# Kernel optimization log

Measured on AMD Instinct MI355X. Metric: run time of the kernel, lower is better.

## Reference

```python
import jax, jax.numpy as jnp
import numpy as np

MASK_RADIUS = 30.0

def _lowpass_mask(H, W):
    cht, cwt = H // 2, W // 2
    fy = jnp.arange(H, dtype=jnp.float32)[:, None]
    fx = jnp.arange(W, dtype=jnp.float32)[None, :]
    dist = jnp.sqrt((fx - cwt) ** 2 + (fy - cht) ** 2)
    return (dist <= MASK_RADIUS).astype(jnp.float32)

def setup_inputs() -> dict:
    key = jax.random.key(0)
    k1, k2, k3 = jax.random.split(key, 3)
    x = jax.random.normal(k1, (16, 64, 128, 128), dtype=jnp.float32)
    weight = jax.random.normal(k2, (64, 64, 3, 3), dtype=jnp.float32)
    bias = jax.random.normal(k3, (64,), dtype=jnp.float32)
    return {"x": x, "weight": weight, "bias": bias}

def reference(x, weight, bias):
    B, Cin, H, W = x.shape
    # torch.fft.fftshift default shifts ALL dims; jnp default matches.
    fft_x = jnp.fft.fftshift(jnp.fft.fft2(x))                    # [B,Cin,H,W] complex
    kernel_fft = jnp.fft.fftshift(jnp.fft.fft2(weight, s=(H, W)))  # [Cout,Cin,H,W] complex
    # low-pass filter in the shifted frequency domain
    fft_x = fft_x * _lowpass_mask(H, W)
    # channel mixing = batched complex GEMM per frequency (avoids [B,Cout,Cin,H,W] intermediate)
    fft_out = jnp.einsum('bihw,oihw->bohw', fft_x, kernel_fft)
    out = jnp.fft.ifft2(jnp.fft.ifftshift(fft_out, axes=(-2, -1)), axes=(-2, -1)).real
    return out + bias[None, :, None, None]
```

## Files before the change

### kernel.cpp

```cpp
#include <hip/hip_runtime.h>


#define PI2_128 0.04908738521234052f
#define NF 1891

typedef __attribute__((ext_vector_type(8))) short bf16x8;
typedef __attribute__((ext_vector_type(4))) float f32x4;

__device__ const int k_flist[64] = {
    2, 6, 10, 14, 18, 22, 26, 30, 34, 38, 42, 46, 50, 54, 58,
    3, 7, 11, 15, 19, 23, 27, 31, 35, 39, 43, 47, 51, 55, 59,
    0, 4, 8, 12, 16, 20, 24, 28, 32, 36, 40, 44, 48, 52, 56, 60,
    1, 5, 9, 13, 17, 21, 25, 29, 33, 37, 41, 45, 49, 53, 57,
    0, 0, 0};

__device__ inline unsigned bf16_rne(float v) {
  unsigned u = __float_as_uint(v);
  return (u + 0x7FFFu + ((u >> 16) & 1u)) >> 16;
}

__device__ inline bf16x8 mk_bf16x8(unsigned a, unsigned b, unsigned c, unsigned d) {
  union { unsigned u[4]; bf16x8 v; } x;
  x.u[0] = a; x.u[1] = b; x.u[2] = c; x.u[3] = d;
  return x.v;
}

__global__ __launch_bounds__(256) void k0_what(const float* __restrict__ w,
                                               unsigned* __restrict__ Wt) {
  const int tid = threadIdx.x;
  const int fxp = blockIdx.x >> 4;
  const int ig = blockIdx.x & 15;
  const int il = tid & 3;
  const int o = ((tid >> 5) << 3) | ((tid >> 2) & 7);
  const int i = ig * 4 + il;
  const int op = (o + 32) & 63;
  const float* wp = w + (size_t)(op * 64 + i) * 9;
  float w9[9];
#pragma unroll
  for (int k = 0; k < 9; ++k) w9[k] = wp[k];

  const float fx = (float)(fxp - 30);
  float sn, cs;
  __sincosf(fx * PI2_128, &sn, &cs);
  const float e1x = cs, e1y = -sn;
  const float e2x = e1x * e1x - e1y * e1y, e2y = 2.f * e1x * e1y;
  float rxr[3], rxi[3];
#pragma unroll
  for (int ky = 0; ky < 3; ++ky) {
    rxr[ky] = w9[ky * 3] + w9[ky * 3 + 1] * e1x + w9[ky * 3 + 2] * e2x;
    rxi[ky] = w9[ky * 3 + 1] * e1y + w9[ky * 3 + 2] * e2y;
  }
  float pyx = 1.f, pyy = 0.f;
  const float stx = 0.9987954562f, sty = -0.04906767433f;
  unsigned* Wb = Wt + (size_t)(fxp * 31) * 4096 + (o >> 3) * 512 + (i >> 4) * 128 +
                 (((i >> 2) & 3) * 8 + (o & 7)) * 4 + (i & 3);
  for (int fy = 0; fy < 31; ++fy) {
    float p2x = pyx * pyx - pyy * pyy, p2y = 2.f * pyx * pyy;
    float Wre = rxr[0] + (rxr[1] * pyx - rxi[1] * pyy) + (rxr[2] * p2x - rxi[2] * p2y);
    float Wim = rxi[0] + (rxr[1] * pyy + rxi[1] * pyx) + (rxr[2] * p2y + rxi[2] * p2x);
    Wb[(size_t)fy * 4096] = bf16_rne(Wre) | (bf16_rne(Wim) << 16);
    float nx = pyx * stx - pyy * sty;
    pyy = pyx * sty + pyy * stx;
    pyx = nx;
  }
}

__global__ __launch_bounds__(256) void k12_fwd(const float* __restrict__ x,
                                               float* __restrict__ X2) {
  __shared__ __align__(16) float Cls[8968];
  const int bi = blockIdx.x;
  const int tid = threadIdx.x;
  const float* img = x + (size_t)bi * 16384;

  {
    const int tg = tid >> 5;
    const int xg = tid & 31;
    const int t_[4] = {4 * tg, 4 * tg + 2, 2 * tg + 1, 2 * tg + 17};
    const float sgn = (tg & 1) ? 1.f : -1.f;
    float pc[4], ps[4], stc[4], sts[4];
#pragma unroll
    for (int f = 0; f < 4; ++f) {
      __sincosf((float)t_[f] * PI2_128, &sts[f], &stc[f]);
      pc[f] = 1.f;
      ps[f] = 0.f;
    }
    float ar_[4][4] = {{0.f}}, ai_[4][4] = {{0.f}};
    for (int y = 0; y < 32; ++y) {
      float v[4][4];
#pragma unroll
      for (int k = 0; k < 4; ++k)
#pragma unroll
        for (int m = 0; m < 4; ++m) v[k][m] = img[(y + 32 * k) * 128 + xg + 32 * m];
#pragma unroll
      for (int m = 0; m < 4; ++m) {
        float s = v[0][m] + v[2][m], d = v[0][m] - v[2][m];
        float s2 = v[1][m] + v[3][m], d2 = (v[1][m] - v[3][m]) * sgn;
        float a0 = s + s2, a1 = s - s2;
        ar_[0][m] += a0 * pc[0];
        ai_[0][m] -= a0 * ps[0];
        ar_[1][m] += a1 * pc[1];
        ai_[1][m] -= a1 * ps[1];
        ar_[2][m] += d * pc[2] + d2 * ps[2];
        ai_[2][m] += -d * ps[2] + d2 * pc[2];
        ar_[3][m] += d * pc[3] + d2 * ps[3];
        ai_[3][m] += -d * ps[3] + d2 * pc[3];
      }
#pragma unroll
      for (int f = 0; f < 4; ++f) {
        float c = pc[f], s = ps[f];
        pc[f] = c * stc[f] - s * sts[f];
        ps[f] = s * stc[f] + c * sts[f];
      }
    }
#pragma unroll
    for (int f = 0; f < 4; ++f) {
      int t = t_[f];
      float Ar = ar_[f][0] + ar_[f][2], Ai = ai_[f][0] + ai_[f][2];
      float Br = ar_[f][0] - ar_[f][2], Bi = ai_[f][0] - ai_[f][2];
      float Cr = ar_[f][1] + ar_[f][3], Ci = ai_[f][1] + ai_[f][3];
      float Dr = ar_[f][1] - ar_[f][3], Di = ai_[f][1] - ai_[f][3];
      float* base = Cls + xg * 70 + 2 * t;
      *(float2*)(base + 0 * 2244) = make_float2(Ar + Cr, Ai + Ci);
      *(float2*)(base + 1 * 2244) = make_float2(Br + Di, Bi - Dr);
      *(float2*)(base + 2 * 2244) = make_float2(Ar - Cr, Ai - Ci);
      *(float2*)(base + 3 * 2244) = make_float2(Br - Di, Bi + Dr);
    }
  }
  __syncthreads();

  {
    const int tg2 = tid >> 5;
    const int fxg = tid & 31;
    float accr[2][4] = {{0.f}}, acci[2][4] = {{0.f}};
    int fxp_[2], r_[2];
    float pc2[2], ps2[2], stc2[2], sts2[2];
#pragma unroll
    for (int u = 0; u < 2; ++u) {
      fxp_[u] = k_flist[2 * fxg + u];
      r_[u] = (fxp_[u] + 2) & 3;
      float fx = (float)(fxp_[u] - 30);
      __sincosf(fx * PI2_128, &sts2[u], &stc2[u]);
      pc2[u] = 1.f;
      ps2[u] = 0.f;
    }
    for (int xx = 0; xx < 32; ++xx) {
#pragma unroll
      for (int u = 0; u < 2; ++u) {
        const float* bp = Cls + r_[u] * 2244 + xx * 70 + 8 * tg2;
        float2 p0 = *(const float2*)(bp);
        float2 p1 = *(const float2*)(bp + 2);
        float2 p2 = *(const float2*)(bp + 4);
        float2 p3 = *(const float2*)(bp + 6);
        float zr[4] = {p0.x, p1.x, p2.x, p3.x};
        float zi[4] = {p0.y, p1.y, p2.y, p3.y};
        float c = pc2[u], s = ps2[u];
#pragma unroll
        for (int tt = 0; tt < 4; ++tt) {
          accr[u][tt] += zr[tt] * c + zi[tt] * s;
          acci[u][tt] += zi[tt] * c - zr[tt] * s;
        }
        pc2[u] = c * stc2[u] - s * sts2[u];
        ps2[u] = s * stc2[u] + c * sts2[u];
      }
    }
    float2* X2c = (float2*)X2 + (size_t)bi * NF;
#pragma unroll
    for (int u = 0; u < 2; ++u) {
      if (2 * fxg + u >= 61) continue;
      int fxp = fxp_[u], fx = fxp - 30;
#pragma unroll
      for (int tt = 0; tt < 4; ++tt) {
        int t = 4 * tg2 + tt;
        if (t >= 31) continue;
        bool keep = (t * t + fx * fx) <= 900;
        X2c[fxp * 31 + t] =
            keep ? make_float2(accr[u][tt], acci[u][tt]) : make_float2(0.f, 0.f);
      }
    }
  }
}

__global__ __launch_bounds__(256) void k3_mfma(const float* __restrict__ X2,
                                               const unsigned* __restrict__ WtB,
                                               float* __restrict__ F) {
  const int nwg = (int)gridDim.x;
  const int orig = (int)blockIdx.x;
  const int xcd = orig & 7;
  const int q = nwg >> 3, r = nwg & 7;
  const int blk = (xcd < r ? xcd * (q + 1) : r * (q + 1) + (xcd - r) * q) + (orig >> 3);

  const int tid = (int)threadIdx.x;
  const int wv = tid >> 6;
  const int g = blk * 4 + wv;
  const int f2 = g >> 1;
  if (f2 >= NF) return;
  const int half = g & 1;
  const int lane = tid & 63;
  const int m = lane & 15;
  const int lg = lane >> 4;
  const int bs = (m + 8) & 15;
  const int co = m & 1;

  float2 xv[4][4];
  const float2* Xc = (const float2*)X2;
#pragma unroll
  for (int ks = 0; ks < 4; ++ks)
#pragma unroll
    for (int t = 0; t < 4; ++t)
      xv[ks][t] = Xc[(size_t)(bs * 64 + ks * 16 + lg * 4 + t) * NF + f2];

  unsigned ahi[4][4], alo[4][4];
#pragma unroll
  for (int ks = 0; ks < 4; ++ks) {
#pragma unroll
    for (int t = 0; t < 4; ++t) {
      float xr = xv[ks][t].x, xi = xv[ks][t].y;
      unsigned hr = bf16_rne(xr), hi2 = bf16_rne(xi);
      float lr = xr - __uint_as_float(hr << 16);
      float li = xi - __uint_as_float(hi2 << 16);
      ahi[ks][t] = hr | (hi2 << 16);
      alo[ks][t] = bf16_rne(lr) | (bf16_rne(li) << 16);
    }
  }

  f32x4 acc[4];
#pragma unroll
  for (int nt = 0; nt < 4; ++nt) acc[nt] = {0.f, 0.f, 0.f, 0.f};

  const unsigned* Wb =
      WtB + (size_t)f2 * 4096 + half * 2048 + (lg * 8 + (m >> 1)) * 4;
#pragma unroll
  for (int ks = 0; ks < 4; ++ks) {
    bf16x8 bfr[4];
#pragma unroll
    for (int nt = 0; nt < 4; ++nt) {
      uint4 wq = *(const uint4*)(Wb + nt * 512 + ks * 128);
      unsigned b0, b1, b2, b3;
      if (co) {
        b0 = (wq.x >> 16) | (wq.x << 16);
        b1 = (wq.y >> 16) | (wq.y << 16);
        b2 = (wq.z >> 16) | (wq.z << 16);
        b3 = (wq.w >> 16) | (wq.w << 16);
      } else {
        b0 = wq.x ^ 0x80000000u;
        b1 = wq.y ^ 0x80000000u;
        b2 = wq.z ^ 0x80000000u;
        b3 = wq.w ^ 0x80000000u;
      }
      bfr[nt] = mk_bf16x8(b0, b1, b2, b3);
    }
    bf16x8 ah = mk_bf16x8(ahi[ks][0], ahi[ks][1], ahi[ks][2], ahi[ks][3]);
    bf16x8 al = mk_bf16x8(alo[ks][0], alo[ks][1], alo[ks][2], alo[ks][3]);
#pragma unroll
    for (int nt = 0; nt < 4; ++nt)
      acc[nt] = __builtin_amdgcn_mfma_f32_16x16x32_bf16(ah, bfr[nt], acc[nt], 0, 0, 0);
#pragma unroll
    for (int nt = 0; nt < 4; ++nt)
      acc[nt] = __builtin_amdgcn_mfma_f32_16x16x32_bf16(al, bfr[nt], acc[nt], 0, 0, 0);
  }

  float* Fo = F + (size_t)f2 * 2048 + half * 64 + m;
#pragma unroll
  for (int nt = 0; nt < 4; ++nt)
#pragma unroll
    for (int rr = 0; rr < 4; ++rr)
      Fo[(lg * 4 + rr) * 128 + nt * 16] = acc[nt][rr];
}

__global__ __launch_bounds__(256) void k45_out(const float* __restrict__ F,
                                               const float* __restrict__ bias,
                                               float* __restrict__ out) {
  __shared__ __align__(16) float2 tw[128];
  __shared__ __align__(16) float U[61 * 132];
  __shared__ __align__(16) float TF[3904];
  const int b = blockIdx.x >> 6;
  const int o = blockIdx.x & 63;
  const int tid = threadIdx.x;
  float2* Fl = (float2*)TF;
  const float2* Fc = (const float2*)F + (size_t)(b * 64 + o);
  if (tid < 128) {
    float sv, cv;
    __sincosf((float)tid * PI2_128, &sv, &cv);
    tw[tid] = make_float2(cv, sv);
  }
  for (int j = tid; j < NF; j += 256) Fl[j] = Fc[(size_t)j * 1024];
  __syncthreads();

  {
    const int fy = tid & 31;
    const int xg = tid >> 3 >> 2;
    if (fy < 31) {
      float Sr[4][4] = {{0.f}}, Si[4][4] = {{0.f}};
      float pr[4], pi[4], cr[4], ci[4];
#pragma unroll
      for (int j = 0; j < 4; ++j) {
        int xj = 4 * xg + j;
        float2 st = tw[xj];
        cr[j] = st.x;
        ci[j] = st.y;
        float2 p0 = tw[(-30 * xj) & 127];
        pr[j] = p0.x;
        pi[j] = p0.y;
      }
      const float2* Frow = Fl + fy;
      for (int f4 = 0; f4 < 60; f4 += 4) {
#pragma unroll
        for (int ss = 0; ss < 4; ++ss) {
          const int r = (ss + 2) & 3;
          float2 fv = Frow[(f4 + ss) * 31];
#pragma unroll
          for (int j = 0; j < 4; ++j) {
            Sr[r][j] += fv.x * pr[j] - fv.y * pi[j];
            Si[r][j] += fv.x * pi[j] + fv.y * pr[j];
            float np = pr[j] * cr[j] - pi[j] * ci[j];
            pi[j] = pi[j] * cr[j] + pr[j] * ci[j];
            pr[j] = np;
          }
        }
      }
      {
        float2 fv = Frow[60 * 31];
#pragma unroll
        for (int j = 0; j < 4; ++j) {
          Sr[2][j] += fv.x * pr[j] - fv.y * pi[j];
          Si[2][j] += fv.x * pi[j] + fv.y * pr[j];
        }
      }
#pragma unroll
      for (int j = 0; j < 4; ++j) {
        int xj = 4 * xg + j;
        float Er = Sr[0][j] + Sr[2][j], Ei = Si[0][j] + Si[2][j];
        float Fr = Sr[0][j] - Sr[2][j], Fi = Si[0][j] - Si[2][j];
        float Gr = Sr[1][j] + Sr[3][j], Gi = Si[1][j] + Si[3][j];
        float Hr = Sr[1][j] - Sr[3][j], Hi = Si[1][j] - Si[3][j];
        U[fy * 132 + xj] = Er + Gr;
        U[fy * 132 + xj + 32] = Fr - Hi;
        U[fy * 132 + xj + 64] = Er - Gr;
        U[fy * 132 + xj + 96] = Fr + Hi;
        if (fy >= 1) {
          U[(30 + fy) * 132 + xj] = Ei + Gi;
          U[(30 + fy) * 132 + xj + 32] = Fi + Hr;
          U[(30 + fy) * 132 + xj + 64] = Ei - Gi;
          U[(30 + fy) * 132 + xj + 96] = Fi - Hr;
        }
      }
    }
  }
  __syncthreads();
  {
    const float sc1 = 1.f / 16384.f;
    float* T = TF;
    for (int j = tid; j < 61 * 64; j += 256) {
      int c = j >> 6, y = j & 63;
      float val;
      if (c == 0) val = sc1;
      else if (c <= 30) val = 2.f * sc1 * tw[(c * y) & 127].x;
      else val = -2.f * sc1 * tw[((c - 30) * y) & 127].y;
      T[j] = val;
    }
  }
  __syncthreads();
  {
    const float* T = TF;
    const int yg = tid >> 5;
    const int xg = tid & 31;
    const int y0 = yg * 8, x0 = xg * 4;
    float Pa[8][4] = {{0.f}}, Qa[8][4] = {{0.f}};
    for (int c = 0; c < 60; c += 2) {
      float tf0[8], tf1[8], uf0[4], uf1[4];
      *(float4*)&tf0[0] = *(const float4*)(&T[c * 64 + y0]);
      *(float4*)&tf0[4] = *(const float4*)(&T[c * 64 + y0 + 4]);
      *(float4*)&tf1[0] = *(const float4*)(&T[(c + 1) * 64 + y0]);
      *(float4*)&tf1[4] = *(const float4*)(&T[(c + 1) * 64 + y0 + 4]);
      *(float4*)&uf0[0] = *(const float4*)(&U[c * 132 + x0]);
      *(float4*)&uf1[0] = *(const float4*)(&U[(c + 1) * 132 + x0]);
#pragma unroll
      for (int jy = 0; jy < 8; ++jy)
#pragma unroll
        for (int jx = 0; jx < 4; ++jx) {
          Pa[jy][jx] += tf0[jy] * uf0[jx];
          Qa[jy][jx] += tf1[jy] * uf1[jx];
        }
    }
    {
      float tf0[8], uf0[4];
      *(float4*)&tf0[0] = *(const float4*)(&T[60 * 64 + y0]);
      *(float4*)&tf0[4] = *(const float4*)(&T[60 * 64 + y0 + 4]);
      *(float4*)&uf0[0] = *(const float4*)(&U[60 * 132 + x0]);
#pragma unroll
      for (int jy = 0; jy < 8; ++jy)
#pragma unroll
        for (int jx = 0; jx < 4; ++jx) Pa[jy][jx] += tf0[jy] * uf0[jx];
    }
    const float bo_ = bias[o];
    float* op = out + (size_t)(b * 64 + o) * 16384;
#pragma unroll
    for (int jy = 0; jy < 8; ++jy) {
      float4 lo, hi;
      lo.x = Pa[jy][0] + Qa[jy][0] + bo_;
      lo.y = Pa[jy][1] + Qa[jy][1] + bo_;
      lo.z = Pa[jy][2] + Qa[jy][2] + bo_;
      lo.w = Pa[jy][3] + Qa[jy][3] + bo_;
      hi.x = Pa[jy][0] - Qa[jy][0] + bo_;
      hi.y = Pa[jy][1] - Qa[jy][1] + bo_;
      hi.z = Pa[jy][2] - Qa[jy][2] + bo_;
      hi.w = Pa[jy][3] - Qa[jy][3] + bo_;
      *(float4*)(op + (y0 + jy) * 128 + x0) = lo;
      *(float4*)(op + (y0 + jy + 64) * 128 + x0) = hi;
    }
  }
}

extern "C" void kernel_launch(void* const* d_in, const int* in_sizes, int n_in,
                              void* d_out, int out_size, void* d_ws, size_t ws_size,
                              hipStream_t stream) {
  (void)in_sizes; (void)n_in; (void)out_size; (void)ws_size;
  const float* x = (const float*)d_in[0];
  const float* w = (const float*)d_in[1];
  const float* bias = (const float*)d_in[2];
  float* out = (float*)d_out;

  unsigned* Wt = (unsigned*)d_ws;
  float* X2 = (float*)d_ws + 7745536;
  float* F = (float*)d_ws + 11618304;

  k0_what<<<976, 256, 0, stream>>>(w, Wt);
  k12_fwd<<<1024, 256, 0, stream>>>(x, X2);
  k3_mfma<<<946, 256, 0, stream>>>(X2, Wt, F);
  k45_out<<<1024, 256, 0, stream>>>(F, bias, out);
}
```

Measured before the change: 236.0 us.

## Add LDS transpose kernels so the MFMA and output stages read contiguously

Adds two tiled, XOR-swizzled LDS transpose kernels. One turns the forward spectrum into a frequency-major layout so k3_mfma's per-frequency channel loads become contiguous. The other turns the mixed spectrum back to a channel-major layout so k45_out reads each plane linearly instead of with a 1024-element stride. k3_mfma now works in place on its buffer: it keeps every wave alive, puts a block barrier between its loads and its stores, and clamps out-of-range waves. The trade is two extra launches and two extra full read/write passes over the spectrum buffers, in exchange for removing heavily strided gathers.

```diff
diff --git a/kernel.cpp b/kernel.cpp
--- a/kernel.cpp
+++ b/kernel.cpp
@@ -180,9 +180,34 @@
   }
 }
 
-__global__ __launch_bounds__(256) void k3_mfma(const float* __restrict__ X2,
+__global__ __launch_bounds__(256) void ktx(const float2* __restrict__ X2,
+                                           float2* __restrict__ X2T) {
+  __shared__ __align__(16) float2 Ld[4096];
+  const int tid = threadIdx.x;
+  const int tf = blockIdx.x % 30;
+  const int tc = blockIdx.x / 30;
+  const int f2_0 = tf * 64;
+  const int lo = tid & 63, hi = tid >> 6;
+#pragma unroll
+  for (int k = 0; k < 16; ++k) {
+    int c = k * 4 + hi;
+    int bi = (c & 15) * 64 + tc * 4 + (c >> 4);
+    int f2 = f2_0 + lo;
+    float2 v = (f2 < NF) ? X2[(size_t)bi * NF + f2] : make_float2(0.f, 0.f);
+    Ld[(c << 6) | (lo ^ c)] = v;
+  }
+  __syncthreads();
+#pragma unroll
+  for (int k = 0; k < 16; ++k) {
+    int fr = k * 4 + hi;
+    int f2 = f2_0 + fr;
+    if (f2 < NF) X2T[(size_t)f2 * 1024 + tc * 64 + lo] = Ld[(lo << 6) | (fr ^ lo)];
+  }
+}
+
+__global__ __launch_bounds__(256) void k3_mfma(const float* X2T,
                                                const unsigned* __restrict__ WtB,
-                                               float* __restrict__ F) {
+                                               float* F) {
   const int nwg = (int)gridDim.x;
   const int orig = (int)blockIdx.x;
   const int xcd = orig & 7;
@@ -192,8 +217,9 @@
   const int tid = (int)threadIdx.x;
   const int wv = tid >> 6;
   const int g = blk * 4 + wv;
-  const int f2 = g >> 1;
-  if (f2 >= NF) return;
+  const int f2v = g >> 1;
+  const bool valid = f2v < NF;
+  const int f2 = valid ? f2v : NF - 1;
   const int half = g & 1;
   const int lane = tid & 63;
   const int m = lane & 15;
@@ -202,12 +228,14 @@
   const int co = m & 1;
 
   float2 xv[4][4];
-  const float2* Xc = (const float2*)X2;
+  const float2* Xc = (const float2*)X2T;
 #pragma unroll
   for (int ks = 0; ks < 4; ++ks)
 #pragma unroll
     for (int t = 0; t < 4; ++t)
-      xv[ks][t] = Xc[(size_t)(bs * 64 + ks * 16 + lg * 4 + t) * NF + f2];
+      xv[ks][t] = Xc[(size_t)f2 * 1024 + (ks * 16 + lg * 4 + t) * 16 + bs];
+
+  __syncthreads();
 
   unsigned ahi[4][4], alo[4][4];
 #pragma unroll
@@ -259,15 +287,41 @@
       acc[nt] = __builtin_amdgcn_mfma_f32_16x16x32_bf16(al, bfr[nt], acc[nt], 0, 0, 0);
   }
 
-  float* Fo = F + (size_t)f2 * 2048 + half * 64 + m;
-#pragma unroll
-  for (int nt = 0; nt < 4; ++nt)
-#pragma unroll
-    for (int rr = 0; rr < 4; ++rr)
-      Fo[(lg * 4 + rr) * 128 + nt * 16] = acc[nt][rr];
-}
-
-__global__ __launch_bounds__(256) void k45_out(const float* __restrict__ F,
+  if (valid) {
+    float* Fo = F + (size_t)f2 * 2048 + half * 64 + m;
+#pragma unroll
+    for (int nt = 0; nt < 4; ++nt)
+#pragma unroll
+      for (int rr = 0; rr < 4; ++rr)
+        Fo[(lg * 4 + rr) * 128 + nt * 16] = acc[nt][rr];
+  }
+}
+
+__global__ __launch_bounds__(256) void ktf(const float2* __restrict__ F2,
+                                           float2* __restrict__ FT) {
+  __shared__ __align__(16) float2 Ld[4096];
+  const int tid = threadIdx.x;
+  const int tf = blockIdx.x % 30;
+  const int tc = blockIdx.x / 30;
+  const int f2_0 = tf * 64, c0 = tc * 64;
+  const int lo = tid & 63, hi = tid >> 6;
+#pragma unroll
+  for (int k = 0; k < 16; ++k) {
+    int fr = k * 4 + hi;
+    int f2 = f2_0 + fr;
+    float2 v = (f2 < NF) ? F2[(size_t)f2 * 1024 + c0 + lo] : make_float2(0.f, 0.f);
+    Ld[(fr << 6) | (lo ^ fr)] = v;
+  }
+  __syncthreads();
+#pragma unroll
+  for (int k = 0; k < 16; ++k) {
+    int cc = k * 4 + hi;
+    int f2 = f2_0 + lo;
+    if (f2 < NF) FT[(size_t)(c0 + cc) * NF + f2] = Ld[(lo << 6) | (cc ^ lo)];
+  }
+}
+
+__global__ __launch_bounds__(256) void k45_out(const float* __restrict__ FT,
                                                const float* __restrict__ bias,
                                                float* __restrict__ out) {
   __shared__ __align__(16) float2 tw[128];
@@ -277,13 +331,13 @@
   const int o = blockIdx.x & 63;
   const int tid = threadIdx.x;
   float2* Fl = (float2*)TF;
-  const float2* Fc = (const float2*)F + (size_t)(b * 64 + o);
+  const float2* Fc = (const float2*)FT + (size_t)(b * 64 + o) * NF;
   if (tid < 128) {
     float sv, cv;
     __sincosf((float)tid * PI2_128, &sv, &cv);
     tw[tid] = make_float2(cv, sv);
   }
-  for (int j = tid; j < NF; j += 256) Fl[j] = Fc[(size_t)j * 1024];
+  for (int j = tid; j < NF; j += 256) Fl[j] = Fc[j];
   __syncthreads();
 
   {
@@ -421,11 +475,13 @@
   float* out = (float*)d_out;
 
   unsigned* Wt = (unsigned*)d_ws;
-  float* X2 = (float*)d_ws + 7745536;
-  float* F = (float*)d_ws + 11618304;
+  float* A = (float*)d_ws + 7745536;
+  float* B = (float*)d_ws + 11618304;
 
   k0_what<<<976, 256, 0, stream>>>(w, Wt);
-  k12_fwd<<<1024, 256, 0, stream>>>(x, X2);
-  k3_mfma<<<946, 256, 0, stream>>>(X2, Wt, F);
-  k45_out<<<1024, 256, 0, stream>>>(F, bias, out);
-}
+  k12_fwd<<<1024, 256, 0, stream>>>(x, A);
+  ktx<<<480, 256, 0, stream>>>((const float2*)A, (float2*)B);
+  k3_mfma<<<946, 256, 0, stream>>>(B, Wt, B);
+  ktf<<<480, 256, 0, stream>>>((const float2*)B, (float2*)A);
+  k45_out<<<1024, 256, 0, stream>>>(A, bias, out);
+}
```

Result: faster. 226.3 us (-4.1%).
